# Optimization experiments

Measured on AMD Instinct MI355X. Metric: run time of the kernel, lower is better.

## Reference

```python
import jax, jax.numpy as jnp
import numpy as np

B, T, D, H, OUT = 256, 512, 64, 512, 1


def _lstm_layer(x, w_ih, w_hh, b_ih, b_hh):
    """Single LSTM layer, batch_first x: [B, T, Din] -> [B, T, H].
    PyTorch gate order: i, f, g, o. gates = x@W_ih^T + b_ih + h@W_hh^T + b_hh.
    """
    Bx = x.shape[0]
    Hh = w_hh.shape[1]
    # Precompute input projection for all timesteps (one big GEMM).
    x_proj = jnp.einsum('btd,gd->btg', x, w_ih) + b_ih + b_hh  # [B, T, 4H]

    def step(carry, xp_t):
        h, c = carry
        gates = xp_t + h @ w_hh.T  # [B, 4H]
        i, f, g, o = jnp.split(gates, 4, axis=-1)
        i = jax.nn.sigmoid(i)
        f = jax.nn.sigmoid(f)
        g = jnp.tanh(g)
        o = jax.nn.sigmoid(o)
        c = f * c + i * g
        h = o * jnp.tanh(c)
        return (h, c), h

    h0 = jnp.zeros((Bx, Hh), dtype=x.dtype)
    c0 = jnp.zeros((Bx, Hh), dtype=x.dtype)
    (_, _), hs = jax.lax.scan(step, (h0, c0), jnp.swapaxes(x_proj, 0, 1))  # hs: [T, B, H]
    return jnp.swapaxes(hs, 0, 1)  # [B, T, H]


def setup_inputs() -> dict:
    key = jax.random.key(0)
    ks = jax.random.split(key, 12)
    s = 1.0 / np.sqrt(H)  # torch LSTM init: U(-1/sqrt(H), 1/sqrt(H))
    u = lambda k, shape: jax.random.uniform(k, shape, jnp.float32, -s, s)
    return {
        'x': jax.random.normal(ks[0], (B, T, D), dtype=jnp.float32),
        'w_ih_0': u(ks[1], (4 * H, D)),
        'w_hh_0': u(ks[2], (4 * H, H)),
        'b_ih_0': u(ks[3], (4 * H,)),
        'b_hh_0': u(ks[4], (4 * H,)),
        'w_ih_1': u(ks[5], (4 * H, H)),
        'w_hh_1': u(ks[6], (4 * H, H)),
        'b_ih_1': u(ks[7], (4 * H,)),
        'b_hh_1': u(ks[8], (4 * H,)),
        'w_fc': u(ks[9], (OUT, H)),
        'b_fc': u(ks[10], (OUT,)),
    }


def reference(x, w_ih_0, w_hh_0, b_ih_0, b_hh_0,
              w_ih_1, w_hh_1, b_ih_1, b_hh_1, w_fc, b_fc):
    h = _lstm_layer(x, w_ih_0, w_hh_0, b_ih_0, b_hh_0)   # layer 0
    h = _lstm_layer(h, w_ih_1, w_hh_1, b_ih_1, b_hh_1)   # layer 1
    last = h[:, -1, :]                                   # [B, H]
    return last @ w_fc.T + b_fc                          # [B, OUT]
```

## Files before the change

### kernel.cpp

```cpp
#include <hip/hip_runtime.h>


typedef _Float16 f16;
typedef _Float16 f16x8 __attribute__((ext_vector_type(8)));
typedef _Float16 f16x4 __attribute__((ext_vector_type(4)));
typedef float    f32x4 __attribute__((ext_vector_type(4)));
typedef unsigned long long u64;

#define T_STEPS 512
#define NBATCH  256
#define DIN     64
#define NHID    512
#define GB      16
#define CBLK    32
#define NGRP2   16
#define NROWS   64
#define HS      (NHID + 8)
#define XS      (DIN + 8)
#define FSTRIDE 32

__device__ __forceinline__ f32x4 mfma16(f16x8 a, f16x8 b, f32x4 c) {
    return __builtin_amdgcn_mfma_f32_16x16x32_f16(a, b, c, 0, 0, 0);
}

__device__ __forceinline__ f16x8 cvt8(const float* p) {
    const float4 v0 = *reinterpret_cast<const float4*>(p);
    const float4 v1 = *reinterpret_cast<const float4*>(p + 4);
    f16x8 r;
    r[0] = (f16)v0.x; r[1] = (f16)v0.y; r[2] = (f16)v0.z; r[3] = (f16)v0.w;
    r[4] = (f16)v1.x; r[5] = (f16)v1.y; r[6] = (f16)v1.z; r[7] = (f16)v1.w;
    return r;
}

__device__ __forceinline__ void act4(const f32x4 gv, const int gate,
                                     float* cc, float* hh)
{
#pragma unroll
    for (int jj = 0; jj < 4; ++jj) {
        const float v  = gv[jj];
        const float xs = (gate == 2) ? 2.0f * v : v;
        const float ee = exp2f(-1.44269504f * xs);
        const float sg = 1.0f / (1.0f + ee);
        const float a  = (gate == 2) ? (2.0f * sg - 1.0f) : sg;
        const float a1 = __shfl_xor(a, 1, 64);
        const float a2 = __shfl_xor(a, 2, 64);
        const float a3 = __shfl_xor(a, 3, 64);
        int d;
        float vi, vf, vg, vo;
        d = gate;     vi = d == 0 ? a : d == 1 ? a1 : d == 2 ? a2 : a3;
        d = gate ^ 1; vf = d == 0 ? a : d == 1 ? a1 : d == 2 ? a2 : a3;
        d = gate ^ 2; vg = d == 0 ? a : d == 1 ? a1 : d == 2 ? a2 : a3;
        d = gate ^ 3; vo = d == 0 ? a : d == 1 ? a1 : d == 2 ? a2 : a3;
        const float cn = vf * cc[jj] + vi * vg;
        cc[jj] = cn;
        const float e2 = exp2f(-2.88539008f * cn);
        const float th = 2.0f / (1.0f + e2) - 1.0f;
        hh[jj] = vo * th;
    }
}

__global__ __launch_bounds__(512, 2) void lstm_fused(
    const f16*  __restrict__ xpk,
    const float* __restrict__ wih0, const float* __restrict__ whh0,
    const float* __restrict__ bih0, const float* __restrict__ bhh0,
    const float* __restrict__ wih1, const float* __restrict__ whh1,
    const float* __restrict__ bih1, const float* __restrict__ bhh1,
    f16* __restrict__ hbuf0,
    f16* __restrict__ hbuf1,
    float* __restrict__ hlast,
    unsigned* flags0, unsigned* flags1)
{
    __shared__ f16 hT0A[GB * HS], hT0B[GB * HS];
    __shared__ f16 hT1A[GB * HS], hT1B[GB * HS];
    __shared__ f16 xTile[2][3][GB * XS];
    __shared__ f16 hs0[2][2][GB * 16];
    __shared__ f16 hs1[2][2][GB * 16];
    __shared__ float Lb0[NROWS], Lb1[NROWS];
    __shared__ unsigned pubcnt[2][2][2];

    const int tid = threadIdx.x;
    const int pid = blockIdx.x & 7;
    const int jb  = blockIdx.x >> 3;
    const int gA  = pid * 2, gB_ = pid * 2 + 1;
    const int bbA = gA * GB, bbB = gB_ * GB;

    if (tid < 8) reinterpret_cast<unsigned*>(pubcnt)[tid] = 0u;
    if (tid < NROWS) {
        const int gr = (tid & 3) * NHID + jb * 16 + (tid >> 2);
        Lb0[tid] = bih0[gr] + bhh0[gr];
        Lb1[tid] = bih1[gr] + bhh1[gr];
    }

    const int w    = tid >> 6;
    const int eng  = w >> 2;
    const int wr   = w & 3;
    const int l    = tid & 63;
    const int col  = l & 15;
    const int q    = l >> 4;
    const int q8   = q << 3;
    const int n    = (wr << 4) | col;
    const int gate = n & 3;
    const int hl   = n >> 2;
    const int grow = (n & 3) * NHID + jb * 16 + (n >> 2);
    const int rb   = (wr << 2) | (l & 3);
    const int rc   = l >> 2;

    f16x8 BWx[16], BWh[16];
    if (eng == 0) {
        const float* sx = wih0 + (size_t)grow * DIN + q8;
#pragma unroll
        for (int s = 0; s < 2; ++s) BWx[s] = cvt8(sx + s * 32);
        const float* sh = whh0 + (size_t)grow * NHID + q8;
#pragma unroll
        for (int s = 0; s < 16; ++s) BWh[s] = cvt8(sh + s * 32);
    } else {
        const float* sx = wih1 + (size_t)grow * NHID + q8;
#pragma unroll
        for (int s = 0; s < 16; ++s) BWx[s] = cvt8(sx + s * 32);
        const float* sh = whh1 + (size_t)grow * NHID + q8;
#pragma unroll
        for (int s = 0; s < 16; ++s) BWh[s] = cvt8(sh + s * 32);
    }
    __syncthreads();
    const float bias_n = (eng == 0) ? Lb0[n] : Lb1[n];

    float cA[4] = {0,0,0,0}, cB[4] = {0,0,0,0};

    auto pollf = [&](const unsigned* flg, int grp, int sp) {
        const unsigned target = (unsigned)(sp + 1);
        const unsigned* fp = flg + (size_t)(grp * CBLK + (l & 31)) * FSTRIDE;
        unsigned spins = 0;
        for (;;) {
            unsigned v = 0xFFFFFFFFu;
            if (l < CBLK)
                v = __hip_atomic_load(fp, __ATOMIC_RELAXED, __HIP_MEMORY_SCOPE_AGENT);
            if (__all(v >= target)) break;
            __builtin_amdgcn_s_sleep(2);
            if (++spins > (1u << 15)) break;
        }
        asm volatile("" ::: "memory");
    };

    auto ldissue = [&](u64* r, const f16* hb, int par, int bb) {
        const u64* src = reinterpret_cast<const u64*>(
            hb + (size_t)par * (NBATCH * NHID) + (size_t)(bb + rb) * NHID) + rc * 8;
#pragma unroll
        for (int j = 0; j < 8; ++j)
            r[j] = __hip_atomic_load(src + j, __ATOMIC_RELAXED, __HIP_MEMORY_SCOPE_AGENT);
    };
    auto tilewr = [&](f16* t, const u64* r) {
        f16* dst = t + rb * HS + rc * 32;
#pragma unroll
        for (int j = 0; j < 8; ++j)
            *reinterpret_cast<u64*>(dst + j * 4) = r[j];
    };

    auto pubwave = [&](f16* hb, unsigned* flg, int grp, int bb, const f16* hsrc,
                       int sp, int eci, int cci) {
        asm volatile("s_waitcnt lgkmcnt(0)" ::: "memory");
        if (l < GB) {
            const u64 v8 = *reinterpret_cast<const u64*>(hsrc + l * 16 + wr * 4);
            u64* dst = reinterpret_cast<u64*>(
                hb + (size_t)(sp & 1) * (NBATCH * NHID)
                   + (size_t)(bb + l) * NHID + jb * 16 + wr * 4);
            __hip_atomic_store(dst, v8, __ATOMIC_RELAXED, __HIP_MEMORY_SCOPE_AGENT);
        }
        asm volatile("s_waitcnt vmcnt(0)" ::: "memory");
        if (l == 0) {
            const unsigned old = atomicAdd(&pubcnt[eci][cci][sp & 1], 1u);
            if (old == 3u) {
                pubcnt[eci][cci][sp & 1] = 0u;
                __hip_atomic_store(flg + (size_t)(grp * CBLK + jb) * FSTRIDE,
                                   (unsigned)(sp + 1),
                                   __ATOMIC_RELAXED, __HIP_MEMORY_SCOPE_AGENT);
            }
        }
    };

    auto comp0 = [&](const f16* xp, const f16* t0, float* cc, f16* hst,
                     int grp, int bb, int s_, bool doh, int cci) {
        f32x4 e0 = {bias_n, bias_n, bias_n, bias_n};
        f32x4 o0 = {0,0,0,0};
#pragma unroll
        for (int k = 0; k < 2; ++k) {
            const f16x8 a0 = *reinterpret_cast<const f16x8*>(xp + col * XS + (q + 4*k) * 8);
            if (k & 1) o0 = mfma16(a0, BWx[k], o0); else e0 = mfma16(a0, BWx[k], e0);
        }
        if (doh) {
#pragma unroll
            for (int k = 0; k < 16; ++k) {
                const f16x8 a0 = *reinterpret_cast<const f16x8*>(t0 + col * HS + (q + 4*k) * 8);
                if (k & 1) o0 = mfma16(a0, BWh[k], o0); else e0 = mfma16(a0, BWh[k], e0);
            }
        }
        const f32x4 gv = e0 + o0;
        float hv[4];
        act4(gv, gate, cc, hv);
        if (gate == 0) {
#pragma unroll
            for (int jj = 0; jj < 4; ++jj)
                hst[(q * 4 + jj) * 16 + hl] = (f16)hv[jj];
        }
        pubwave(hbuf0, flags0, grp, bb, hst, s_, 0, cci);
    };

    auto comp1 = [&](const f16* t0, const f16* t1, float* cc, f16* hst,
                     int grp, int bb, int sp_, bool doh2, bool last, int cci) {
        f32x4 e0 = {bias_n, bias_n, bias_n, bias_n};
        f32x4 o0 = {0,0,0,0};
#pragma unroll
        for (int k = 0; k < 16; ++k) {
            const f16x8 a0 = *reinterpret_cast<const f16x8*>(t0 + col * HS + (q + 4*k) * 8);
            if (k & 1) o0 = mfma16(a0, BWx[k], o0); else e0 = mfma16(a0, BWx[k], e0);
        }
        if (doh2) {
#pragma unroll
            for (int k = 0; k < 16; ++k) {
                const f16x8 a0 = *reinterpret_cast<const f16x8*>(t1 + col * HS + (q + 4*k) * 8);
                if (k & 1) o0 = mfma16(a0, BWh[k], o0); else e0 = mfma16(a0, BWh[k], e0);
            }
        }
        const f32x4 gv = e0 + o0;
        float hv[4];
        act4(gv, gate, cc, hv);
        if (last) {
            if (gate == 0) {
#pragma unroll
                for (int jj = 0; jj < 4; ++jj)
                    hlast[(size_t)(bb + q * 4 + jj) * NHID + jb * 16 + hl] = hv[jj];
            }
        } else {
            if (gate == 0) {
#pragma unroll
                for (int jj = 0; jj < 4; ++jj)
                    hst[(q * 4 + jj) * 16 + hl] = (f16)hv[jj];
            }
            pubwave(hbuf1, flags1, grp, bb, hst, sp_, 1, cci);
        }
    };

    if (eng == 0) {
#pragma unroll
        for (int t0 = 0; t0 < 2; ++t0) {
            const u64 vA = *reinterpret_cast<const u64*>(
                xpk + ((size_t)t0 * NBATCH + bbA + rb) * DIN + rc * 4);
            const u64 vB = *reinterpret_cast<const u64*>(
                xpk + ((size_t)t0 * NBATCH + bbB + rb) * DIN + rc * 4);
            *reinterpret_cast<u64*>(xTile[0][t0] + rb * XS + rc * 4) = vA;
            *reinterpret_cast<u64*>(xTile[1][t0] + rb * XS + rc * 4) = vB;
        }
    }
    __syncthreads();

    u64 rA[8], rB[8];
    for (int s = 0; s <= T_STEPS; ++s) {
        const bool doh0 = (s >= 1);
        const bool doh1 = (s >= 2);
        if (eng == 0) {
            if (doh0) { pollf(flags0, gA, s - 1); ldissue(rA, hbuf0, (s - 1) & 1, bbA); tilewr(hT0A, rA); }
        } else {
            if (doh1) { pollf(flags1, gA, s - 2); ldissue(rA, hbuf1, (s - 2) & 1, bbA); tilewr(hT1A, rA); }
        }
        __syncthreads();
        if (eng == 0) {
            if (doh0) { pollf(flags0, gB_, s - 1); ldissue(rB, hbuf0, (s - 1) & 1, bbB); }
        } else {
            if (doh1) { pollf(flags1, gB_, s - 2); ldissue(rB, hbuf1, (s - 2) & 1, bbB); }
        }
        if (eng == 0) {
            if (s < T_STEPS)
                comp0(xTile[0][s % 3], hT0A, cA, hs0[0][s & 1], gA, bbA, s, doh0, 0);
        } else {
            if (s >= 1)
                comp1(hT0A, hT1A, cA, hs1[0][(s - 1) & 1], gA, bbA, s - 1, doh1,
                      s == T_STEPS, 0);
        }
        if (eng == 0) { if (doh0) tilewr(hT0B, rB); }
        else          { if (doh1) tilewr(hT1B, rB); }
        __syncthreads();
        if (eng == 0) {
            if (s < T_STEPS)
                comp0(xTile[1][s % 3], hT0B, cB, hs0[1][s & 1], gB_, bbB, s, doh0, 1);
            if (s + 2 < T_STEPS) {
                const u64 vA = *reinterpret_cast<const u64*>(
                    xpk + ((size_t)(s + 2) * NBATCH + bbA + rb) * DIN + rc * 4);
                const u64 vB = *reinterpret_cast<const u64*>(
                    xpk + ((size_t)(s + 2) * NBATCH + bbB + rb) * DIN + rc * 4);
                *reinterpret_cast<u64*>(xTile[0][(s + 2) % 3] + rb * XS + rc * 4) = vA;
                *reinterpret_cast<u64*>(xTile[1][(s + 2) % 3] + rb * XS + rc * 4) = vB;
            }
        } else {
            if (s >= 1)
                comp1(hT0B, hT1B, cB, hs1[1][(s - 1) & 1], gB_, bbB, s - 1, doh1,
                      s == T_STEPS, 1);
        }
        __syncthreads();
    }
}

__global__ void pack_x(const float* __restrict__ xin, f16* __restrict__ xp) {
    const int i = blockIdx.x * 256 + threadIdx.x;
    const long long e = (long long)i * 4;
    const int d = (int)(e & (DIN - 1));
    const int b = (int)((e >> 6) & (NBATCH - 1));
    const int t = (int)(e >> 14);
    if (t < T_STEPS) {
        const float4 v = *reinterpret_cast<const float4*>(
            xin + ((size_t)b * T_STEPS + t) * DIN + d);
        f16x4 o;
        o[0] = (f16)v.x; o[1] = (f16)v.y; o[2] = (f16)v.z; o[3] = (f16)v.w;
        *reinterpret_cast<f16x4*>(xp + ((size_t)t * NBATCH + b) * DIN + d) = o;
    }
}

__global__ void fc_kernel(const float* __restrict__ hlast, const float* __restrict__ wfc,
                          const float* __restrict__ bfc, float* __restrict__ out) {
    const int wv = threadIdx.x >> 6, l = threadIdx.x & 63;
    const int b  = blockIdx.x * 4 + wv;
    const float* hr = hlast + b * NHID;
    float s = 0.f;
#pragma unroll
    for (int j = 0; j < 8; ++j) s += hr[l + 64 * j] * wfc[l + 64 * j];
#pragma unroll
    for (int off = 32; off; off >>= 1) s += __shfl_xor(s, off, 64);
    if (l == 0) out[b] = s + bfc[0];
}

extern "C" void kernel_launch(void* const* d_in, const int* in_sizes, int n_in,
                              void* d_out, int out_size, void* d_ws, size_t ws_size,
                              hipStream_t stream) {
    const float* x    = (const float*)d_in[0];
    const float* wih0 = (const float*)d_in[1];
    const float* whh0 = (const float*)d_in[2];
    const float* bih0 = (const float*)d_in[3];
    const float* bhh0 = (const float*)d_in[4];
    const float* wih1 = (const float*)d_in[5];
    const float* whh1 = (const float*)d_in[6];
    const float* bih1 = (const float*)d_in[7];
    const float* bhh1 = (const float*)d_in[8];
    const float* wfc  = (const float*)d_in[9];
    const float* bfc  = (const float*)d_in[10];
    float* out = (float*)d_out;

    char* ws = (char*)d_ws;
    const size_t XPK_ELEMS  = (size_t)NBATCH * T_STEPS * DIN;
    const size_t FLAG_ELEMS = (size_t)NGRP2 * CBLK * FSTRIDE;
    size_t off = 0;
    f16* xpk = (f16*)(ws + off);        off += XPK_ELEMS * 2;
    f16* hb0 = (f16*)(ws + off);        off += (size_t)2 * NBATCH * NHID * 2;
    f16* hb1 = (f16*)(ws + off);        off += (size_t)2 * NBATCH * NHID * 2;
    float* hlast = (float*)(ws + off);  off += (size_t)NBATCH * NHID * 4;
    unsigned* flg0 = (unsigned*)(ws + off); off += FLAG_ELEMS * 4;
    unsigned* flg1 = (unsigned*)(ws + off); off += FLAG_ELEMS * 4;

    hipMemsetAsync(flg0, 0, 2 * FLAG_ELEMS * 4, stream);

    pack_x<<<(int)(XPK_ELEMS / 4 / 256), 256, 0, stream>>>(x, xpk);

    {
        const f16* in0 = xpk;
        void* a[] = { (void*)&in0,
                      (void*)&wih0, (void*)&whh0, (void*)&bih0, (void*)&bhh0,
                      (void*)&wih1, (void*)&whh1, (void*)&bih1, (void*)&bhh1,
                      (void*)&hb0, (void*)&hb1, (void*)&hlast,
                      (void*)&flg0, (void*)&flg1 };
        hipLaunchCooperativeKernel(lstm_fused, dim3(256), dim3(512), a, 0, stream);
    }

    fc_kernel<<<64, 256, 0, stream>>>(hlast, wfc, bfc, out);
}
```

Before: 4.920 ms.

## Split each block's batch slice into four 8-row chunks with pipelined poll/compute

```diff
diff --git a/kernel.cpp b/kernel.cpp
--- a/kernel.cpp
+++ b/kernel.cpp
@@ -11,9 +11,9 @@
 #define NBATCH  256
 #define DIN     64
 #define NHID    512
-#define GB      16
+#define GB      8
 #define CBLK    32
-#define NGRP2   16
+#define NGRP4   32
 #define NROWS   64
 #define HS      (NHID + 8)
 #define XS      (DIN + 8)
@@ -70,21 +70,20 @@
     float* __restrict__ hlast,
     unsigned* flags0, unsigned* flags1)
 {
-    __shared__ f16 hT0A[GB * HS], hT0B[GB * HS];
-    __shared__ f16 hT1A[GB * HS], hT1B[GB * HS];
-    __shared__ f16 xTile[2][3][GB * XS];
-    __shared__ f16 hs0[2][2][GB * 16];
-    __shared__ f16 hs1[2][2][GB * 16];
+    __shared__ f16 hT0[4][GB * HS];
+    __shared__ f16 hT1[4][GB * HS];
+    __shared__ f16 xTile[4][3][GB * XS];
+    __shared__ f16 hs0[4][GB * 16];
+    __shared__ f16 hs1[4][GB * 16];
     __shared__ float Lb0[NROWS], Lb1[NROWS];
-    __shared__ unsigned pubcnt[2][2][2];
+    __shared__ unsigned pubcnt[2][2];
 
     const int tid = threadIdx.x;
     const int pid = blockIdx.x & 7;
     const int jb  = blockIdx.x >> 3;
-    const int gA  = pid * 2, gB_ = pid * 2 + 1;
-    const int bbA = gA * GB, bbB = gB_ * GB;
-
-    if (tid < 8) reinterpret_cast<unsigned*>(pubcnt)[tid] = 0u;
+    const int bbP = pid * 32;
+
+    if (tid < 4) reinterpret_cast<unsigned*>(pubcnt)[tid] = 0u;
     if (tid < NROWS) {
         const int gr = (tid & 3) * NHID + jb * 16 + (tid >> 2);
         Lb0[tid] = bih0[gr] + bhh0[gr];
@@ -96,14 +95,15 @@
     const int wr   = w & 3;
     const int l    = tid & 63;
     const int col  = l & 15;
+    const int colc = col & (GB - 1);
     const int q    = l >> 4;
     const int q8   = q << 3;
     const int n    = (wr << 4) | col;
     const int gate = n & 3;
     const int hl   = n >> 2;
     const int grow = (n & 3) * NHID + jb * 16 + (n >> 2);
-    const int rb   = (wr << 2) | (l & 3);
-    const int rc   = l >> 2;
+    const int rb8  = (wr << 1) | (l & 1);
+    const int rc8  = l >> 1;
 
     f16x8 BWx[16], BWh[16];
     if (eng == 0) {
@@ -124,7 +124,8 @@
     __syncthreads();
     const float bias_n = (eng == 0) ? Lb0[n] : Lb1[n];
 
-    float cA[4] = {0,0,0,0}, cB[4] = {0,0,0,0};
+    float cc0[4][4] = {{0,0,0,0},{0,0,0,0},{0,0,0,0},{0,0,0,0}};
+    float cc1[4][4] = {{0,0,0,0},{0,0,0,0},{0,0,0,0},{0,0,0,0}};
 
     auto pollf = [&](const unsigned* flg, int grp, int sp) {
         const unsigned target = (unsigned)(sp + 1);
@@ -143,156 +144,149 @@
 
     auto ldissue = [&](u64* r, const f16* hb, int par, int bb) {
         const u64* src = reinterpret_cast<const u64*>(
-            hb + (size_t)par * (NBATCH * NHID) + (size_t)(bb + rb) * NHID) + rc * 8;
-#pragma unroll
-        for (int j = 0; j < 8; ++j)
+            hb + (size_t)par * (NBATCH * NHID) + (size_t)(bb + rb8) * NHID) + rc8 * 4;
+#pragma unroll
+        for (int j = 0; j < 4; ++j)
             r[j] = __hip_atomic_load(src + j, __ATOMIC_RELAXED, __HIP_MEMORY_SCOPE_AGENT);
     };
     auto tilewr = [&](f16* t, const u64* r) {
-        f16* dst = t + rb * HS + rc * 32;
-#pragma unroll
-        for (int j = 0; j < 8; ++j)
+        f16* dst = t + rb8 * HS + rc8 * 16;
+#pragma unroll
+        for (int j = 0; j < 4; ++j)
             *reinterpret_cast<u64*>(dst + j * 4) = r[j];
     };
 
-    auto pubwave = [&](f16* hb, unsigned* flg, int grp, int bb, const f16* hsrc,
-                       int sp, int eci, int cci) {
+    auto puball = [&](f16* hb, unsigned* flg, f16 (*hsarr)[GB * 16], int sp, int eci) {
         asm volatile("s_waitcnt lgkmcnt(0)" ::: "memory");
         if (l < GB) {
-            const u64 v8 = *reinterpret_cast<const u64*>(hsrc + l * 16 + wr * 4);
-            u64* dst = reinterpret_cast<u64*>(
-                hb + (size_t)(sp & 1) * (NBATCH * NHID)
-                   + (size_t)(bb + l) * NHID + jb * 16 + wr * 4);
-            __hip_atomic_store(dst, v8, __ATOMIC_RELAXED, __HIP_MEMORY_SCOPE_AGENT);
+#pragma unroll
+            for (int c = 0; c < 4; ++c) {
+                const u64 v8 = *reinterpret_cast<const u64*>(&hsarr[c][l * 16 + wr * 4]);
+                u64* dst = reinterpret_cast<u64*>(
+                    hb + (size_t)(sp & 1) * (NBATCH * NHID)
+                       + (size_t)(bbP + c * GB + l) * NHID + jb * 16 + wr * 4);
+                __hip_atomic_store(dst, v8, __ATOMIC_RELAXED, __HIP_MEMORY_SCOPE_AGENT);
+            }
         }
         asm volatile("s_waitcnt vmcnt(0)" ::: "memory");
         if (l == 0) {
-            const unsigned old = atomicAdd(&pubcnt[eci][cci][sp & 1], 1u);
+            const unsigned old = atomicAdd(&pubcnt[eci][sp & 1], 1u);
             if (old == 3u) {
-                pubcnt[eci][cci][sp & 1] = 0u;
-                __hip_atomic_store(flg + (size_t)(grp * CBLK + jb) * FSTRIDE,
-                                   (unsigned)(sp + 1),
-                                   __ATOMIC_RELAXED, __HIP_MEMORY_SCOPE_AGENT);
-            }
-        }
-    };
-
-    auto comp0 = [&](const f16* xp, const f16* t0, float* cc, f16* hst,
-                     int grp, int bb, int s_, bool doh, int cci) {
+                pubcnt[eci][sp & 1] = 0u;
+#pragma unroll
+                for (int c = 0; c < 4; ++c)
+                    __hip_atomic_store(
+                        flg + (size_t)((pid * 4 + c) * CBLK + jb) * FSTRIDE,
+                        (unsigned)(sp + 1),
+                        __ATOMIC_RELAXED, __HIP_MEMORY_SCOPE_AGENT);
+            }
+        }
+    };
+
+    auto xstage = [&](int tt) {
+        const int row = l & 7;
+        const int cb  = l >> 3;
+#pragma unroll
+        for (int j = 0; j < 2; ++j) {
+            const u64 v = *reinterpret_cast<const u64*>(
+                xpk + ((size_t)tt * NBATCH + bbP + wr * GB + row) * DIN + (cb * 2 + j) * 4);
+            *reinterpret_cast<u64*>(&xTile[wr][tt % 3][row * XS + (cb * 2 + j) * 4]) = v;
+        }
+    };
+
+    auto comp0 = [&](int c, int s_) {
+        const f16* xp = &xTile[c][s_ % 3][0];
         f32x4 e0 = {bias_n, bias_n, bias_n, bias_n};
-        f32x4 o0 = {0,0,0,0};
+        f32x4 o0 = {0, 0, 0, 0};
 #pragma unroll
         for (int k = 0; k < 2; ++k) {
-            const f16x8 a0 = *reinterpret_cast<const f16x8*>(xp + col * XS + (q + 4*k) * 8);
+            const f16x8 a0 = *reinterpret_cast<const f16x8*>(xp + colc * XS + (q + 4*k) * 8);
             if (k & 1) o0 = mfma16(a0, BWx[k], o0); else e0 = mfma16(a0, BWx[k], e0);
         }
-        if (doh) {
+        if (s_ >= 1) {
+            const f16* t0 = &hT0[c][0];
 #pragma unroll
             for (int k = 0; k < 16; ++k) {
-                const f16x8 a0 = *reinterpret_cast<const f16x8*>(t0 + col * HS + (q + 4*k) * 8);
+                const f16x8 a0 = *reinterpret_cast<const f16x8*>(t0 + colc * HS + (q + 4*k) * 8);
                 if (k & 1) o0 = mfma16(a0, BWh[k], o0); else e0 = mfma16(a0, BWh[k], e0);
             }
         }
         const f32x4 gv = e0 + o0;
         float hv[4];
-        act4(gv, gate, cc, hv);
-        if (gate == 0) {
+        act4(gv, gate, cc0[c], hv);
+        if (gate == 0 && q < 2) {
 #pragma unroll
             for (int jj = 0; jj < 4; ++jj)
-                hst[(q * 4 + jj) * 16 + hl] = (f16)hv[jj];
-        }
-        pubwave(hbuf0, flags0, grp, bb, hst, s_, 0, cci);
-    };
-
-    auto comp1 = [&](const f16* t0, const f16* t1, float* cc, f16* hst,
-                     int grp, int bb, int sp_, bool doh2, bool last, int cci) {
+                hs0[c][(q * 4 + jj) * 16 + hl] = (f16)hv[jj];
+        }
+    };
+
+    auto comp1 = [&](int c, int sp) {
         f32x4 e0 = {bias_n, bias_n, bias_n, bias_n};
-        f32x4 o0 = {0,0,0,0};
+        f32x4 o0 = {0, 0, 0, 0};
+        const f16* t0 = &hT0[c][0];
 #pragma unroll
         for (int k = 0; k < 16; ++k) {
-            const f16x8 a0 = *reinterpret_cast<const f16x8*>(t0 + col * HS + (q + 4*k) * 8);
+            const f16x8 a0 = *reinterpret_cast<const f16x8*>(t0 + colc * HS + (q + 4*k) * 8);
             if (k & 1) o0 = mfma16(a0, BWx[k], o0); else e0 = mfma16(a0, BWx[k], e0);
         }
-        if (doh2) {
+        if (sp >= 1) {
+            const f16* t1 = &hT1[c][0];
 #pragma unroll
             for (int k = 0; k < 16; ++k) {
-                const f16x8 a0 = *reinterpret_cast<const f16x8*>(t1 + col * HS + (q + 4*k) * 8);
+                const f16x8 a0 = *reinterpret_cast<const f16x8*>(t1 + colc * HS + (q + 4*k) * 8);
                 if (k & 1) o0 = mfma16(a0, BWh[k], o0); else e0 = mfma16(a0, BWh[k], e0);
             }
         }
         const f32x4 gv = e0 + o0;
         float hv[4];
-        act4(gv, gate, cc, hv);
-        if (last) {
-            if (gate == 0) {
+        act4(gv, gate, cc1[c], hv);
+        if (sp == T_STEPS - 1) {
+            if (gate == 0 && q < 2) {
 #pragma unroll
                 for (int jj = 0; jj < 4; ++jj)
-                    hlast[(size_t)(bb + q * 4 + jj) * NHID + jb * 16 + hl] = hv[jj];
-            }
-        } else {
-            if (gate == 0) {
-#pragma unroll
-                for (int jj = 0; jj < 4; ++jj)
-                    hst[(q * 4 + jj) * 16 + hl] = (f16)hv[jj];
-            }
-            pubwave(hbuf1, flags1, grp, bb, hst, sp_, 1, cci);
-        }
-    };
-
-    if (eng == 0) {
-#pragma unroll
-        for (int t0 = 0; t0 < 2; ++t0) {
-            const u64 vA = *reinterpret_cast<const u64*>(
-                xpk + ((size_t)t0 * NBATCH + bbA + rb) * DIN + rc * 4);
-            const u64 vB = *reinterpret_cast<const u64*>(
-                xpk + ((size_t)t0 * NBATCH + bbB + rb) * DIN + rc * 4);
-            *reinterpret_cast<u64*>(xTile[0][t0] + rb * XS + rc * 4) = vA;
-            *reinterpret_cast<u64*>(xTile[1][t0] + rb * XS + rc * 4) = vB;
-        }
-    }
+                    hlast[(size_t)(bbP + c * GB + q * 4 + jj) * NHID + jb * 16 + hl] = hv[jj];
+            }
+        } else if (gate == 0 && q < 2) {
+#pragma unroll
+            for (int jj = 0; jj < 4; ++jj)
+                hs1[c][(q * 4 + jj) * 16 + hl] = (f16)hv[jj];
+        }
+    };
+
+    if (eng == 0) { xstage(0); xstage(1); }
     __syncthreads();
 
-    u64 rA[8], rB[8];
+    u64 r4[4];
     for (int s = 0; s <= T_STEPS; ++s) {
         const bool doh0 = (s >= 1);
         const bool doh1 = (s >= 2);
+#pragma unroll
+        for (int p = 0; p < 4; ++p) {
+            const int grp = pid * 4 + p;
+            const int bb  = grp * GB;
+            if (eng == 0) {
+                if (doh0) { pollf(flags0, grp, s - 1); ldissue(r4, hbuf0, (s - 1) & 1, bb); }
+                if (p == 0 && s + 2 < T_STEPS) xstage(s + 2);
+                if (p >= 1 && s < T_STEPS) comp0(p - 1, s);
+                if (doh0) tilewr(&hT0[p][0], r4);
+            } else {
+                if (doh1) { pollf(flags1, grp, s - 2); ldissue(r4, hbuf1, (s - 2) & 1, bb); }
+                if (p >= 1 && s >= 1) comp1(p - 1, s - 1);
+                if (doh1) tilewr(&hT1[p][0], r4);
+            }
+            __syncthreads();
+        }
         if (eng == 0) {
-            if (doh0) { pollf(flags0, gA, s - 1); ldissue(rA, hbuf0, (s - 1) & 1, bbA); tilewr(hT0A, rA); }
+            if (s < T_STEPS) {
+                comp0(3, s);
+                puball(hbuf0, flags0, hs0, s, 0);
+            }
         } else {
-            if (doh1) { pollf(flags1, gA, s - 2); ldissue(rA, hbuf1, (s - 2) & 1, bbA); tilewr(hT1A, rA); }
-        }
-        __syncthreads();
-        if (eng == 0) {
-            if (doh0) { pollf(flags0, gB_, s - 1); ldissue(rB, hbuf0, (s - 1) & 1, bbB); }
-        } else {
-            if (doh1) { pollf(flags1, gB_, s - 2); ldissue(rB, hbuf1, (s - 2) & 1, bbB); }
-        }
-        if (eng == 0) {
-            if (s < T_STEPS)
-                comp0(xTile[0][s % 3], hT0A, cA, hs0[0][s & 1], gA, bbA, s, doh0, 0);
-        } else {
-            if (s >= 1)
-                comp1(hT0A, hT1A, cA, hs1[0][(s - 1) & 1], gA, bbA, s - 1, doh1,
-                      s == T_STEPS, 0);
-        }
-        if (eng == 0) { if (doh0) tilewr(hT0B, rB); }
-        else          { if (doh1) tilewr(hT1B, rB); }
-        __syncthreads();
-        if (eng == 0) {
-            if (s < T_STEPS)
-                comp0(xTile[1][s % 3], hT0B, cB, hs0[1][s & 1], gB_, bbB, s, doh0, 1);
-            if (s + 2 < T_STEPS) {
-                const u64 vA = *reinterpret_cast<const u64*>(
-                    xpk + ((size_t)(s + 2) * NBATCH + bbA + rb) * DIN + rc * 4);
-                const u64 vB = *reinterpret_cast<const u64*>(
-                    xpk + ((size_t)(s + 2) * NBATCH + bbB + rb) * DIN + rc * 4);
-                *reinterpret_cast<u64*>(xTile[0][(s + 2) % 3] + rb * XS + rc * 4) = vA;
-                *reinterpret_cast<u64*>(xTile[1][(s + 2) % 3] + rb * XS + rc * 4) = vB;
-            }
-        } else {
-            if (s >= 1)
-                comp1(hT0B, hT1B, cB, hs1[1][(s - 1) & 1], gB_, bbB, s - 1, doh1,
-                      s == T_STEPS, 1);
+            if (s >= 1) {
+                comp1(3, s - 1);
+                if (s < T_STEPS) puball(hbuf1, flags1, hs1, s - 1, 1);
+            }
         }
         __syncthreads();
     }
@@ -344,7 +338,7 @@
 
     char* ws = (char*)d_ws;
     const size_t XPK_ELEMS  = (size_t)NBATCH * T_STEPS * DIN;
-    const size_t FLAG_ELEMS = (size_t)NGRP2 * CBLK * FSTRIDE;
+    const size_t FLAG_ELEMS = (size_t)NGRP4 * CBLK * FSTRIDE;
     size_t off = 0;
     f16* xpk = (f16*)(ws + off);        off += XPK_ELEMS * 2;
     f16* hb0 = (f16*)(ws + off);        off += (size_t)2 * NBATCH * NHID * 2;
```

Measured after the change: 6.811 ms. +38.4%, slower.

## Merge flag polls for both batch groups and prefetch hidden state a step early

Applied to the files above, without the earlier changes.

```diff
diff --git a/kernel.cpp b/kernel.cpp
--- a/kernel.cpp
+++ b/kernel.cpp
@@ -126,14 +126,14 @@
 
     float cA[4] = {0,0,0,0}, cB[4] = {0,0,0,0};
 
-    auto pollf = [&](const unsigned* flg, int grp, int sp) {
+    auto poll2 = [&](const unsigned* flg, int sp) {
         const unsigned target = (unsigned)(sp + 1);
+        const int grp = (l < 32) ? gA : gB_;
         const unsigned* fp = flg + (size_t)(grp * CBLK + (l & 31)) * FSTRIDE;
         unsigned spins = 0;
         for (;;) {
-            unsigned v = 0xFFFFFFFFu;
-            if (l < CBLK)
-                v = __hip_atomic_load(fp, __ATOMIC_RELAXED, __HIP_MEMORY_SCOPE_AGENT);
+            const unsigned v = __hip_atomic_load(fp, __ATOMIC_RELAXED,
+                                                 __HIP_MEMORY_SCOPE_AGENT);
             if (__all(v >= target)) break;
             __builtin_amdgcn_s_sleep(2);
             if (++spins > (1u << 15)) break;
@@ -239,60 +239,52 @@
         }
     };
 
-    if (eng == 0) {
-#pragma unroll
-        for (int t0 = 0; t0 < 2; ++t0) {
-            const u64 vA = *reinterpret_cast<const u64*>(
-                xpk + ((size_t)t0 * NBATCH + bbA + rb) * DIN + rc * 4);
-            const u64 vB = *reinterpret_cast<const u64*>(
-                xpk + ((size_t)t0 * NBATCH + bbB + rb) * DIN + rc * 4);
-            *reinterpret_cast<u64*>(xTile[0][t0] + rb * XS + rc * 4) = vA;
-            *reinterpret_cast<u64*>(xTile[1][t0] + rb * XS + rc * 4) = vB;
-        }
-    }
+    auto xstage = [&](int tt) {
+        const u64 vA = *reinterpret_cast<const u64*>(
+            xpk + ((size_t)tt * NBATCH + bbA + rb) * DIN + rc * 4);
+        const u64 vB = *reinterpret_cast<const u64*>(
+            xpk + ((size_t)tt * NBATCH + bbB + rb) * DIN + rc * 4);
+        *reinterpret_cast<u64*>(xTile[0][tt % 3] + rb * XS + rc * 4) = vA;
+        *reinterpret_cast<u64*>(xTile[1][tt % 3] + rb * XS + rc * 4) = vB;
+    };
+
+    if (eng == 0) { xstage(0); xstage(1); }
     __syncthreads();
 
     u64 rA[8], rB[8];
     for (int s = 0; s <= T_STEPS; ++s) {
-        const bool doh0 = (s >= 1);
-        const bool doh1 = (s >= 2);
-        if (eng == 0) {
-            if (doh0) { pollf(flags0, gA, s - 1); ldissue(rA, hbuf0, (s - 1) & 1, bbA); tilewr(hT0A, rA); }
-        } else {
-            if (doh1) { pollf(flags1, gA, s - 2); ldissue(rA, hbuf1, (s - 2) & 1, bbA); tilewr(hT1A, rA); }
-        }
-        __syncthreads();
-        if (eng == 0) {
-            if (doh0) { pollf(flags0, gB_, s - 1); ldissue(rB, hbuf0, (s - 1) & 1, bbB); }
-        } else {
-            if (doh1) { pollf(flags1, gB_, s - 2); ldissue(rB, hbuf1, (s - 2) & 1, bbB); }
-        }
-        if (eng == 0) {
-            if (s < T_STEPS)
-                comp0(xTile[0][s % 3], hT0A, cA, hs0[0][s & 1], gA, bbA, s, doh0, 0);
-        } else {
-            if (s >= 1)
-                comp1(hT0A, hT1A, cA, hs1[0][(s - 1) & 1], gA, bbA, s - 1, doh1,
-                      s == T_STEPS, 0);
-        }
-        if (eng == 0) { if (doh0) tilewr(hT0B, rB); }
-        else          { if (doh1) tilewr(hT1B, rB); }
+        if (eng == 0) { if (s >= 1) tilewr(hT0A, rA); }
+        else          { if (s >= 2) tilewr(hT1A, rA); }
         __syncthreads();
         if (eng == 0) {
             if (s < T_STEPS)
-                comp0(xTile[1][s % 3], hT0B, cB, hs0[1][s & 1], gB_, bbB, s, doh0, 1);
-            if (s + 2 < T_STEPS) {
-                const u64 vA = *reinterpret_cast<const u64*>(
-                    xpk + ((size_t)(s + 2) * NBATCH + bbA + rb) * DIN + rc * 4);
-                const u64 vB = *reinterpret_cast<const u64*>(
-                    xpk + ((size_t)(s + 2) * NBATCH + bbB + rb) * DIN + rc * 4);
-                *reinterpret_cast<u64*>(xTile[0][(s + 2) % 3] + rb * XS + rc * 4) = vA;
-                *reinterpret_cast<u64*>(xTile[1][(s + 2) % 3] + rb * XS + rc * 4) = vB;
-            }
+                comp0(xTile[0][s % 3], hT0A, cA, hs0[0][s & 1], gA, bbA, s, s >= 1, 0);
+            if (s >= 1) tilewr(hT0B, rB);
         } else {
             if (s >= 1)
-                comp1(hT0B, hT1B, cB, hs1[1][(s - 1) & 1], gB_, bbB, s - 1, doh1,
+                comp1(hT0A, hT1A, cA, hs1[0][(s - 1) & 1], gA, bbA, s - 1, s >= 2,
+                      s == T_STEPS, 0);
+            if (s >= 2) tilewr(hT1B, rB);
+        }
+        __syncthreads();
+        if (eng == 0) {
+            if (s < T_STEPS) {
+                comp0(xTile[1][s % 3], hT0B, cB, hs0[1][s & 1], gB_, bbB, s, s >= 1, 1);
+                poll2(flags0, s);
+                ldissue(rA, hbuf0, s & 1, bbA);
+                ldissue(rB, hbuf0, s & 1, bbB);
+            }
+            if (s + 2 < T_STEPS) xstage(s + 2);
+        } else {
+            if (s >= 1) {
+                comp1(hT0B, hT1B, cB, hs1[1][(s - 1) & 1], gB_, bbB, s - 1, s >= 2,
                       s == T_STEPS, 1);
+                if (s < T_STEPS) {
+                    poll2(flags1, s - 1);
+                    ldissue(rA, hbuf1, (s - 1) & 1, bbA);
+                    ldissue(rB, hbuf1, (s - 1) & 1, bbB);
+                }
+            }
         }
         __syncthreads();
     }
```

Result: slower. 6.146 ms (+24.9%).
